# Performance work log

Hardware: AMD Instinct MI355X
Metric: run time of the kernel (lower is better)

The kernel has to match this reference:

```python
import jax, jax.numpy as jnp
import numpy as np

D_MODEL = 2048
NUM_HEADS = 32
D_HEAD = D_MODEL // NUM_HEADS
L = 2048


def setup_inputs() -> dict:
    key = jax.random.key(0)
    ks = jax.random.split(key, 9)
    s = 0.02  # init scale
    return {
        "X": jax.random.normal(ks[0], (L, D_MODEL), dtype=jnp.float32),
        "Wq_w": jax.random.normal(ks[1], (D_MODEL, D_MODEL), jnp.float32) * s,
        "Wq_b": jax.random.normal(ks[2], (D_MODEL,), jnp.float32) * s,
        "Wk_w": jax.random.normal(ks[3], (D_MODEL, D_MODEL), jnp.float32) * s,
        "Wk_b": jax.random.normal(ks[4], (D_MODEL,), jnp.float32) * s,
        "Wv_w": jax.random.normal(ks[5], (D_MODEL, D_MODEL), jnp.float32) * s,
        "Wv_b": jax.random.normal(ks[6], (D_MODEL,), jnp.float32) * s,
        "Wo_w": jax.random.normal(ks[7], (D_MODEL, D_MODEL), jnp.float32) * s,
        "Wo_b": jax.random.normal(ks[8], (D_MODEL,), jnp.float32) * s,
    }


def reference(X, Wq_w, Wq_b, Wk_w, Wk_b, Wv_w, Wv_b, Wo_w, Wo_b):
    # torch.nn.Linear: y = x @ W.T + b
    seq = X.shape[0]
    Q = (X @ Wq_w.T + Wq_b).reshape(seq, D_HEAD, NUM_HEADS)  # (L, d, h)
    K = (X @ Wk_w.T + Wk_b).reshape(seq, D_HEAD, NUM_HEADS)
    V = (X @ Wv_w.T + Wv_b).reshape(seq, D_HEAD, NUM_HEADS)
    # scores[l, m, h] = sum_d Q[l,d,h] * K[m,d,h]; note scale is sqrt(d_model),
    # faithful to the source (not sqrt(d_head)).
    scores = jnp.einsum('ldh,mdh->lmh', Q, K) / jnp.sqrt(jnp.float32(D_MODEL))
    attn = jax.nn.softmax(scores, axis=1)  # softmax over key axis m
    out = jnp.einsum('lmh,mdh->ldh', attn, V).reshape(seq, D_MODEL)
    return out @ Wo_w.T + Wo_b
```

## Files before the change

kernel.cpp:

```cpp
#include <hip/hip_runtime.h>
#include <hip/hip_bf16.h>
#include <stdint.h>
#include <stddef.h>

#define L_SEQ   2048
#define DM      2048
#define NH      32
#define DH      64
#define QSCALE  0.02209708691207961f
#define MAT_N   (L_SEQ * DM)

typedef __bf16  bf16x8 __attribute__((ext_vector_type(8)));
typedef float   f32x4  __attribute__((ext_vector_type(4)));
typedef __hip_bfloat16 bf16;

__device__ __forceinline__ void gl_lds16(const bf16* g, bf16* l) {
    __builtin_amdgcn_global_load_lds(
        (const __attribute__((address_space(1))) unsigned int*)g,
        (__attribute__((address_space(3))) unsigned int*)l,
        16, 0, 0);
}

__device__ __forceinline__ void conv8s(const float* src, bf16* dst, int i, float sc) {
    float4 a = *(const float4*)(src + i);
    float4 b = *(const float4*)(src + i + 4);
    union { bf16 h[8]; uint4 u; } pk;
    pk.h[0] = __float2bfloat16(a.x * sc); pk.h[1] = __float2bfloat16(a.y * sc);
    pk.h[2] = __float2bfloat16(a.z * sc); pk.h[3] = __float2bfloat16(a.w * sc);
    pk.h[4] = __float2bfloat16(b.x * sc); pk.h[5] = __float2bfloat16(b.y * sc);
    pk.h[6] = __float2bfloat16(b.z * sc); pk.h[7] = __float2bfloat16(b.w * sc);
    *(uint4*)(dst + i) = pk.u;
}

__global__ __launch_bounds__(256)
void convert4_kernel(const float* __restrict__ s0, const float* __restrict__ s1,
                     const float* __restrict__ s2, const float* __restrict__ s3,
                     bf16* __restrict__ d0, bf16* __restrict__ d1,
                     bf16* __restrict__ d2, bf16* __restrict__ d3)
{
    const float* s; bf16* d; float sc = 1.0f;
    switch (blockIdx.y) {
        case 0:  s = s0; d = d0; break;
        case 1:  s = s1; d = d1; sc = QSCALE; break;
        case 2:  s = s2; d = d2; break;
        default: s = s3; d = d3; break;
    }
    const int i = (blockIdx.x * 256 + threadIdx.x) * 8;
    conv8s(s, d, i, sc);
}

__global__ __launch_bounds__(256)
void convert_wo_perm_kernel(const float* __restrict__ s, bf16* __restrict__ d)
{
    const int t   = blockIdx.x * 256 + threadIdx.x;
    const int row = t >> 8;
    const int k0  = (t & 255) * 8;
    const float* sr = s + (size_t)row * DM;
    union { bf16 h[8]; uint4 u; } pk;
#pragma unroll
    for (int j = 0; j < 8; ++j) {
        const int kp = k0 + j;
        const int k  = ((kp & 63) << 5) | (kp >> 6);
        pk.h[j] = __float2bfloat16(sr[k]);
    }
    *(uint4*)(d + (size_t)row * DM + k0) = pk.u;
}

__global__ __launch_bounds__(512)
void qkv8_gemm_kernel(const bf16* __restrict__ Xb,
                      const bf16* __restrict__ Wq, const float* __restrict__ bq,
                      const bf16* __restrict__ Wk, const float* __restrict__ bk,
                      const bf16* __restrict__ Wv, const float* __restrict__ bv,
                      bf16* __restrict__ Qws, bf16* __restrict__ Kws, bf16* __restrict__ Vws)
{
    __shared__ bf16 lds[2 * 32768];

    const int bid = blockIdx.x;
    const int mt  = bid & 7;
    const int nt  = bid >> 3;
    const int m0  = mt << 8;
    const int ng0 = nt << 8;
    const int z   = ng0 >> 11;
    const int n0  = ng0 & 2047;
    const bf16*  W    = (z == 0) ? Wq : (z == 1) ? Wk : Wv;
    const float* bias = (z == 0) ? bq : (z == 1) ? bk : bv;

    const int tid  = threadIdx.x;
    const int lane = tid & 63;
    const int wave = tid >> 6;
    const int wm   = wave >> 2;
    const int wn   = wave & 3;
    const int grp8 = (lane >> 4) * 8;
    const int grp4 = (lane >> 4) * 4;
    const int l15  = lane & 15;
    const int axor = (l15 & 7) << 3;

    const int scol = ((tid & 7) * 8) ^ (((tid >> 3) & 7) << 3);
    const bf16* gb[8];
    int loff[8];
#pragma unroll
    for (int e = 0; e < 8; ++e) {
        const int hh  = e >> 1;
        const int row = (e & 1) * 64 + (tid >> 3);
        loff[e] = hh * 8192 + (e & 1) * 4096 + tid * 8;
        if (hh < 2) {
            gb[e] = Xb + (size_t)(m0 + hh * 128 + row) * DM + scol;
        } else {
            const int nn   = n0 + (hh - 2) * 128 + row;
            const int brow = ((nn & 63) << 5) | (nn >> 6);
            gb[e] = W + (size_t)brow * DM + scol;
        }
    }

    const bool swap  = (z == 2);
    const int  aside = swap ? 16384 : 0;
    const int  bside = swap ? 0 : 16384;
    const bf16* fa0 = lds + aside + wm * 8192 + l15 * 64;
    const bf16* fb0 = lds + bside + (wn >> 1) * 8192 + ((wn & 1) * 64 + l15) * 64;

    f32x4 acc[8][4];
    const f32x4 zero = {0.f, 0.f, 0.f, 0.f};
#pragma unroll
    for (int i = 0; i < 8; ++i)
#pragma unroll
        for (int j = 0; j < 4; ++j) acc[i][j] = zero;

#pragma unroll
    for (int e = 0; e < 8; ++e) gl_lds16(gb[e],      lds + loff[e]);
#pragma unroll
    for (int e = 0; e < 8; ++e) gl_lds16(gb[e] + 64, lds + 32768 + loff[e]);
    asm volatile("s_waitcnt vmcnt(8)" ::: "memory");
    asm volatile("s_barrier" ::: "memory");

    for (int t = 0; t < 32; ++t) {
        const int cb = (t & 1) << 15;
        const bf16* fa = fa0 + cb;
        const bf16* fb = fb0 + cb;
        const int c0 = grp8 ^ axor;
        const int c1 = (32 + grp8) ^ axor;

        bf16x8 af[8], bfr[4];
#pragma unroll
        for (int i = 0; i < 8; ++i) af[i] = *(const bf16x8*)(fa + i * 1024 + c0);
#pragma unroll
        for (int j = 0; j < 4; ++j) bfr[j] = *(const bf16x8*)(fb + j * 1024 + c0);
        asm volatile("s_barrier" ::: "memory");
        __builtin_amdgcn_s_setprio(1);
#pragma unroll
        for (int i = 0; i < 8; ++i)
#pragma unroll
            for (int j = 0; j < 4; ++j)
                acc[i][j] = __builtin_amdgcn_mfma_f32_16x16x32_bf16(af[i], bfr[j], acc[i][j], 0, 0, 0);
        __builtin_amdgcn_s_setprio(0);

#pragma unroll
        for (int i = 0; i < 8; ++i) af[i] = *(const bf16x8*)(fa + i * 1024 + c1);
#pragma unroll
        for (int j = 0; j < 4; ++j) bfr[j] = *(const bf16x8*)(fb + j * 1024 + c1);
        asm volatile("s_waitcnt lgkmcnt(0)" ::: "memory");
        asm volatile("s_barrier" ::: "memory");
        if (t + 2 < 32) {
            const int kb2 = (t + 2) << 6;
#pragma unroll
            for (int e = 0; e < 8; ++e)
                gl_lds16(gb[e] + kb2, lds + cb + loff[e]);
            asm volatile("s_waitcnt vmcnt(8)" ::: "memory");
        } else if (t == 30) {
            asm volatile("s_waitcnt vmcnt(0)" ::: "memory");
        }
        __builtin_amdgcn_s_setprio(1);
#pragma unroll
        for (int i = 0; i < 8; ++i)
#pragma unroll
            for (int j = 0; j < 4; ++j)
                acc[i][j] = __builtin_amdgcn_mfma_f32_16x16x32_bf16(af[i], bfr[j], acc[i][j], 0, 0, 0);
        __builtin_amdgcn_s_setprio(0);
        asm volatile("s_barrier" ::: "memory");
    }

    if (z == 0) {
#pragma unroll
        for (int j = 0; j < 4; ++j) {
            const int np = n0 + wn * 64 + j * 16 + l15;
            const float bb = bias[((np & 63) << 5) | (np >> 6)] * QSCALE;
            const size_t base = ((size_t)(np >> 6) * L_SEQ) * DH + (np & 63);
#pragma unroll
            for (int i = 0; i < 8; ++i)
#pragma unroll
                for (int r = 0; r < 4; ++r) {
                    const int m = m0 + wm * 128 + i * 16 + grp4 + r;
                    Qws[base + (size_t)m * DH] = __float2bfloat16(acc[i][j][r] + bb);
                }
        }
    } else if (z == 1) {
#pragma unroll
        for (int j = 0; j < 4; ++j) {
            const int np = n0 + wn * 64 + j * 16 + l15;
            const float bb = bias[((np & 63) << 5) | (np >> 6)];
            const size_t base = ((size_t)(np >> 6) * L_SEQ) * DH + (np & 63);
#pragma unroll
            for (int i = 0; i < 8; ++i)
#pragma unroll
                for (int r = 0; r < 4; ++r) {
                    const int m = m0 + wm * 128 + i * 16 + grp4 + r;
                    Kws[base + (size_t)m * DH] = __float2bfloat16(acc[i][j][r] + bb);
                }
        }
    } else {
#pragma unroll
        for (int i = 0; i < 8; ++i)
#pragma unroll
            for (int r = 0; r < 4; ++r) {
                const int np = n0 + wm * 128 + i * 16 + grp4 + r;
                const float bb = bias[((np & 63) << 5) | (np >> 6)];
#pragma unroll
                for (int j = 0; j < 4; ++j) {
                    const int mcol = m0 + wn * 64 + j * 16 + l15;
                    Vws[(size_t)np * L_SEQ + mcol] = __float2bfloat16(acc[i][j][r] + bb);
                }
            }
    }
}

template<bool PERM>
__device__ __forceinline__ void gemm_mainloop(const bf16* __restrict__ A,
                                              const bf16* __restrict__ B,
                                              int m0, int n0, int kb0, int kb1,
                                              bf16* lds_a, bf16* lds_b,
                                              const bf16* fa, const bf16* fb,
                                              f32x4 acc[4][4])
{
    const int tid  = threadIdx.x;
    const int lane = tid & 63;
    const int wave = tid >> 6;
    const int wr   = (wave >> 1) * 64;
    const int wc   = (wave & 1) * 64;
    const int grp8 = (lane >> 4) * 8;
    const int l15  = lane & 15;

    for (int kb = kb0; kb < kb1; kb += 64) {
        __syncthreads();
#pragma unroll
        for (int r = 0; r < 4; ++r) {
            const int idx = r * 256 + tid;
            const int row = idx >> 3;
            const int col = (idx & 7) * 8;
            gl_lds16(A + (size_t)(m0 + row) * DM + kb + col, lds_a + idx * 8);
            int brow;
            if (PERM) { const int n = n0 + row; brow = ((n & 63) << 5) | (n >> 6); }
            else      { brow = n0 + row; }
            gl_lds16(B + (size_t)brow * DM + kb + col, lds_b + idx * 8);
        }
        __syncthreads();
#pragma unroll
        for (int ks = 0; ks < 2; ++ks) {
            bf16x8 af[4], bfr[4];
#pragma unroll
            for (int i = 0; i < 4; ++i)
                af[i] = *(const bf16x8*)(fa + (wr + i * 16 + l15) * 64 + ks * 32 + grp8);
#pragma unroll
            for (int j = 0; j < 4; ++j)
                bfr[j] = *(const bf16x8*)(fb + (wc + j * 16 + l15) * 64 + ks * 32 + grp8);
#pragma unroll
            for (int i = 0; i < 4; ++i)
#pragma unroll
                for (int j = 0; j < 4; ++j)
                    acc[i][j] = __builtin_amdgcn_mfma_f32_16x16x32_bf16(af[i], bfr[j], acc[i][j], 0, 0, 0);
        }
    }
}

__global__ __launch_bounds__(256)
void out_gemm_splitk_kernel(const bf16* __restrict__ A,
                            const bf16* __restrict__ Wo,
                            float* __restrict__ P0, float* __restrict__ P1)
{
    __shared__ bf16 lds_a[128 * 64];
    __shared__ bf16 lds_b[128 * 64];
    const int m0 = blockIdx.y * 128, n0 = blockIdx.x * 128;
    const int kz = blockIdx.z;
    float* P = kz ? P1 : P0;

    const f32x4 zero = {0.f, 0.f, 0.f, 0.f};
    f32x4 acc[4][4];
#pragma unroll
    for (int i = 0; i < 4; ++i)
#pragma unroll
        for (int j = 0; j < 4; ++j) acc[i][j] = zero;

    gemm_mainloop<false>(A, Wo, m0, n0, kz * (DM / 2), kz * (DM / 2) + DM / 2,
                         lds_a, lds_b, lds_a, lds_b, acc);

    const int lane = threadIdx.x & 63;
    const int wave = threadIdx.x >> 6;
    const int wr = (wave >> 1) * 64, wc = (wave & 1) * 64;
    const int grp4 = (lane >> 4) * 4, l15 = lane & 15;

#pragma unroll
    for (int j = 0; j < 4; ++j) {
        const int n = n0 + wc + j * 16 + l15;
#pragma unroll
        for (int i = 0; i < 4; ++i) {
#pragma unroll
            for (int r = 0; r < 4; ++r) {
                const int m = m0 + wr + i * 16 + grp4 + r;
                P[(size_t)m * DM + n] = acc[i][j][r];
            }
        }
    }
}

__global__ __launch_bounds__(256)
void bias_sum_kernel(const float* __restrict__ P0, const float* __restrict__ P1,
                     const float* __restrict__ bo, float* __restrict__ out)
{
    const int i = (blockIdx.x * 256 + threadIdx.x) * 4;
    float4 a = *(const float4*)(P0 + i);
    float4 b = *(const float4*)(P1 + i);
    float4 c = *(const float4*)(bo + (i & (DM - 1)));
    float4 o;
    o.x = a.x + b.x + c.x; o.y = a.y + b.y + c.y;
    o.z = a.z + b.z + c.z; o.w = a.w + b.w + c.w;
    *(float4*)(out + i) = o;
}

__global__ __launch_bounds__(256)
void attention_kernel(const bf16* __restrict__ Qws,
                      const bf16* __restrict__ Kws,
                      const bf16* __restrict__ Vws,
                      bf16* __restrict__ Attn)
{
    __shared__ bf16 Klds[64 * 72];
    __shared__ bf16 Vlds[64 * 72];
    __shared__ bf16 Plds[64 * 72];

    const int h = blockIdx.x, qb = blockIdx.y;
    const int tid = threadIdx.x;
    const int wave = tid >> 6;
    const int lane = tid & 63;
    const int grp = lane >> 4;
    const int l15 = lane & 15;

    const bf16* Qh = Qws + (size_t)h * L_SEQ * DH;
    const bf16* Kh = Kws + (size_t)h * L_SEQ * DH;
    const bf16* Vh = Vws + (size_t)h * DH * L_SEQ;

    const int q0 = qb * 64 + wave * 16;

    bf16x8 qf0 = *(const bf16x8*)(Qh + (size_t)(q0 + l15) * DH + grp * 8);
    bf16x8 qf1 = *(const bf16x8*)(Qh + (size_t)(q0 + l15) * DH + 32 + grp * 8);

    const f32x4 zero = {0.f, 0.f, 0.f, 0.f};
    f32x4 Oacc[4];
#pragma unroll
    for (int t = 0; t < 4; ++t) Oacc[t] = zero;
    float lsum = 0.f;

    for (int kb = 0; kb < L_SEQ / 64; ++kb) {
        __syncthreads();
#pragma unroll
        for (int rr = 0; rr < 2; ++rr) {
            const int idx = rr * 256 + tid;
            const int row = idx >> 3;
            const int col = (idx & 7) * 8;
            uint4 kv = *(const uint4*)(Kh + (size_t)(kb * 64 + row) * DH + col);
            *(uint4*)(&Klds[row * 72 + col]) = kv;
            uint4 vv = *(const uint4*)(Vh + (size_t)row * L_SEQ + kb * 64 + col);
            *(uint4*)(&Vlds[row * 72 + col]) = vv;
        }
        __syncthreads();

#pragma unroll
        for (int t = 0; t < 4; ++t) {
            bf16x8 k0 = *(const bf16x8*)(&Klds[(t * 16 + l15) * 72 + grp * 8]);
            bf16x8 k1 = *(const bf16x8*)(&Klds[(t * 16 + l15) * 72 + 32 + grp * 8]);
            f32x4 s = zero;
            s = __builtin_amdgcn_mfma_f32_16x16x32_bf16(k0, qf0, s, 0, 0, 0);
            s = __builtin_amdgcn_mfma_f32_16x16x32_bf16(k1, qf1, s, 0, 0, 0);
            float p0 = __expf(s[0]), p1 = __expf(s[1]),
                  p2 = __expf(s[2]), p3 = __expf(s[3]);
            lsum += (p0 + p1) + (p2 + p3);
            union { bf16 hh[4]; uint2 u; } pk;
            pk.hh[0] = __float2bfloat16(p0); pk.hh[1] = __float2bfloat16(p1);
            pk.hh[2] = __float2bfloat16(p2); pk.hh[3] = __float2bfloat16(p3);
            *(uint2*)(&Plds[((size_t)wave * 16 + l15) * 72 + t * 16 + grp * 4]) = pk.u;
        }

        asm volatile("s_waitcnt lgkmcnt(0)" ::: "memory");

#pragma unroll
        for (int ks = 0; ks < 2; ++ks) {
            bf16x8 pa = *(const bf16x8*)(&Plds[(wave * 16 + l15) * 72 + ks * 32 + grp * 8]);
#pragma unroll
            for (int t = 0; t < 4; ++t) {
                bf16x8 vb = *(const bf16x8*)(&Vlds[(t * 16 + l15) * 72 + ks * 32 + grp * 8]);
                Oacc[t] = __builtin_amdgcn_mfma_f32_16x16x32_bf16(pa, vb, Oacc[t], 0, 0, 0);
            }
        }
    }

    float s = lsum;
    s += __shfl_xor(s, 16, 64);
    s += __shfl_xor(s, 32, 64);
    const float inv = 1.f / s;
    float invs[4];
#pragma unroll
    for (int r = 0; r < 4; ++r)
        invs[r] = __shfl(inv, grp * 4 + r, 64);

#pragma unroll
    for (int t = 0; t < 4; ++t) {
#pragma unroll
        for (int r = 0; r < 4; ++r) {
            const int m = q0 + grp * 4 + r;
            const int d = t * 16 + l15;
            Attn[(size_t)m * DM + h * 64 + d] = __float2bfloat16(Oacc[t][r] * invs[r]);
        }
    }
}

extern "C" void kernel_launch(void* const* d_in, const int* in_sizes, int n_in,
                              void* d_out, int out_size, void* d_ws, size_t ws_size,
                              hipStream_t stream)
{
    const float* X  = (const float*)d_in[0];
    const float* Wq = (const float*)d_in[1];
    const float* bq = (const float*)d_in[2];
    const float* Wk = (const float*)d_in[3];
    const float* bk = (const float*)d_in[4];
    const float* Wv = (const float*)d_in[5];
    const float* bv = (const float*)d_in[6];
    const float* Wo = (const float*)d_in[7];
    const float* bo = (const float*)d_in[8];
    float* out = (float*)d_out;

    bf16* Xb   = (bf16*)d_ws;
    bf16* Wqb  = Xb  + (size_t)MAT_N;
    bf16* Wkb  = Wqb + (size_t)MAT_N;
    bf16* Wvb  = Wkb + (size_t)MAT_N;
    bf16* Qws  = Wvb + (size_t)MAT_N;
    bf16* Kws  = Qws + (size_t)MAT_N;
    bf16* Vws  = Kws + (size_t)MAT_N;
    bf16* Wob  = Xb;
    bf16* Attn = Wqb;
    float* P0  = (float*)Wkb;
    float* P1  = (float*)Qws;

    convert4_kernel<<<dim3(2048, 4), 256, 0, stream>>>(X, Wq, Wk, Wv, Xb, Wqb, Wkb, Wvb);
    qkv8_gemm_kernel<<<dim3(192), 512, 0, stream>>>(Xb, Wqb, bq, Wkb, bk, Wvb, bv,
                                                    Qws, Kws, Vws);
    convert_wo_perm_kernel<<<dim3(2048), 256, 0, stream>>>(Wo, Wob);
    attention_kernel<<<dim3(32, 32), 256, 0, stream>>>(Qws, Kws, Vws, Attn);
    out_gemm_splitk_kernel<<<dim3(16, 16, 2), 256, 0, stream>>>(Attn, Wob, P0, P1);
    bias_sum_kernel<<<dim3(4096), 256, 0, stream>>>(P0, P1, bo, out);
}
```

Measured before the change: 302.7 us.

## Double-buffer attention and output GEMM with async LDS loads and swizzle

The attention kernel now uses 512-thread blocks covering 128 queries each. It double-buffers K/V tiles through direct global-to-LDS loads with an XOR swizzle in place of padding, and uses exp2 with the log2(e) factor folded into the Q scale. The output GEMM gets the same treatment: a double-buffered, swizzled mainloop with loads issued two tiles ahead and priority hints around the MFMA blocks. The aim is to hide global-load latency and cut LDS bank conflicts and transcendental cost, at the price of more LDS per block and tighter barrier sequencing.

New measurement: 263.8 us. 12.8% less time.

```diff
diff --git a/kernel.cpp b/kernel.cpp
--- a/kernel.cpp
+++ b/kernel.cpp
@@ -8,11 +8,18 @@
 #define NH      32
 #define DH      64
 #define QSCALE  0.02209708691207961f
+#define QS2     0.0318793579f
 #define MAT_N   (L_SEQ * DM)
 
 typedef __bf16  bf16x8 __attribute__((ext_vector_type(8)));
 typedef float   f32x4  __attribute__((ext_vector_type(4)));
 typedef __hip_bfloat16 bf16;
+
+#if __has_builtin(__builtin_amdgcn_exp2f)
+#define EXP2F(x) __builtin_amdgcn_exp2f(x)
+#else
+#define EXP2F(x) __expf((x) * 0.6931471805599453f)
+#endif
 
 __device__ __forceinline__ void gl_lds16(const bf16* g, bf16* l) {
     __builtin_amdgcn_global_load_lds(
@@ -41,7 +48,7 @@
     const float* s; bf16* d; float sc = 1.0f;
     switch (blockIdx.y) {
         case 0:  s = s0; d = d0; break;
-        case 1:  s = s1; d = d1; sc = QSCALE; break;
+        case 1:  s = s1; d = d1; sc = QS2; break;
         case 2:  s = s2; d = d2; break;
         default: s = s3; d = d3; break;
     }
@@ -182,7 +189,7 @@
 #pragma unroll
         for (int j = 0; j < 4; ++j) {
             const int np = n0 + wn * 64 + j * 16 + l15;
-            const float bb = bias[((np & 63) << 5) | (np >> 6)] * QSCALE;
+            const float bb = bias[((np & 63) << 5) | (np >> 6)] * QS2;
             const size_t base = ((size_t)(np >> 6) * L_SEQ) * DH + (np & 63);
 #pragma unroll
             for (int i = 0; i < 8; ++i)
@@ -222,79 +229,96 @@
     }
 }
 
-template<bool PERM>
-__device__ __forceinline__ void gemm_mainloop(const bf16* __restrict__ A,
-                                              const bf16* __restrict__ B,
-                                              int m0, int n0, int kb0, int kb1,
-                                              bf16* lds_a, bf16* lds_b,
-                                              const bf16* fa, const bf16* fb,
-                                              f32x4 acc[4][4])
-{
+__global__ __launch_bounds__(256)
+void out8_gemm_kernel(const bf16* __restrict__ A,
+                      const bf16* __restrict__ Wo,
+                      float* __restrict__ P0, float* __restrict__ P1)
+{
+    __shared__ bf16 lds[2 * 16384];
+
+    const int m0 = blockIdx.y * 128, n0 = blockIdx.x * 128;
+    const int kz = blockIdx.z;
+    float* P = kz ? P1 : P0;
+    const int kbase = kz * 1024;
+
     const int tid  = threadIdx.x;
     const int lane = tid & 63;
     const int wave = tid >> 6;
     const int wr   = (wave >> 1) * 64;
     const int wc   = (wave & 1) * 64;
     const int grp8 = (lane >> 4) * 8;
+    const int grp4 = (lane >> 4) * 4;
     const int l15  = lane & 15;
-
-    for (int kb = kb0; kb < kb1; kb += 64) {
-        __syncthreads();
-#pragma unroll
-        for (int r = 0; r < 4; ++r) {
-            const int idx = r * 256 + tid;
-            const int row = idx >> 3;
-            const int col = (idx & 7) * 8;
-            gl_lds16(A + (size_t)(m0 + row) * DM + kb + col, lds_a + idx * 8);
-            int brow;
-            if (PERM) { const int n = n0 + row; brow = ((n & 63) << 5) | (n >> 6); }
-            else      { brow = n0 + row; }
-            gl_lds16(B + (size_t)brow * DM + kb + col, lds_b + idx * 8);
-        }
-        __syncthreads();
-#pragma unroll
-        for (int ks = 0; ks < 2; ++ks) {
-            bf16x8 af[4], bfr[4];
-#pragma unroll
-            for (int i = 0; i < 4; ++i)
-                af[i] = *(const bf16x8*)(fa + (wr + i * 16 + l15) * 64 + ks * 32 + grp8);
+    const int axor = (l15 & 7) << 3;
+
+    const bf16* gb[8]; int loff[8];
+#pragma unroll
+    for (int e = 0; e < 8; ++e) {
+        const int idx = (e & 3) * 256 + tid;
+        const int row = idx >> 3;
+        const int sc  = ((idx & 7) * 8) ^ ((row & 7) << 3);
+        if (e < 4) { gb[e] = A  + (size_t)(m0 + row) * DM + kbase + sc; loff[e] = idx * 8; }
+        else       { gb[e] = Wo + (size_t)(n0 + row) * DM + kbase + sc; loff[e] = 8192 + idx * 8; }
+    }
+
+    f32x4 acc[4][4];
+    const f32x4 zero = {0.f, 0.f, 0.f, 0.f};
+#pragma unroll
+    for (int i = 0; i < 4; ++i)
+#pragma unroll
+        for (int j = 0; j < 4; ++j) acc[i][j] = zero;
+
+#pragma unroll
+    for (int e = 0; e < 8; ++e) gl_lds16(gb[e],      lds + loff[e]);
+#pragma unroll
+    for (int e = 0; e < 8; ++e) gl_lds16(gb[e] + 64, lds + 16384 + loff[e]);
+    asm volatile("s_waitcnt vmcnt(8)" ::: "memory");
+    asm volatile("s_barrier" ::: "memory");
+
+    for (int t = 0; t < 16; ++t) {
+        const int cb = (t & 1) << 14;
+        const bf16* fa = lds + cb;
+        const bf16* fb = lds + cb + 8192;
+        const int c0 = grp8 ^ axor;
+        const int c1 = (32 + grp8) ^ axor;
+
+        bf16x8 af[4], bfr[4];
+#pragma unroll
+        for (int i = 0; i < 4; ++i) af[i]  = *(const bf16x8*)(fa + (wr + i * 16 + l15) * 64 + c0);
+#pragma unroll
+        for (int j = 0; j < 4; ++j) bfr[j] = *(const bf16x8*)(fb + (wc + j * 16 + l15) * 64 + c0);
+        asm volatile("s_barrier" ::: "memory");
+        __builtin_amdgcn_s_setprio(1);
+#pragma unroll
+        for (int i = 0; i < 4; ++i)
 #pragma unroll
             for (int j = 0; j < 4; ++j)
-                bfr[j] = *(const bf16x8*)(fb + (wc + j * 16 + l15) * 64 + ks * 32 + grp8);
-#pragma unroll
-            for (int i = 0; i < 4; ++i)
-#pragma unroll
-                for (int j = 0; j < 4; ++j)
-                    acc[i][j] = __builtin_amdgcn_mfma_f32_16x16x32_bf16(af[i], bfr[j], acc[i][j], 0, 0, 0);
-        }
-    }
-}
-
-__global__ __launch_bounds__(256)
-void out_gemm_splitk_kernel(const bf16* __restrict__ A,
-                            const bf16* __restrict__ Wo,
-                            float* __restrict__ P0, float* __restrict__ P1)
-{
-    __shared__ bf16 lds_a[128 * 64];
-    __shared__ bf16 lds_b[128 * 64];
-    const int m0 = blockIdx.y * 128, n0 = blockIdx.x * 128;
-    const int kz = blockIdx.z;
-    float* P = kz ? P1 : P0;
-
-    const f32x4 zero = {0.f, 0.f, 0.f, 0.f};
-    f32x4 acc[4][4];
-#pragma unroll
-    for (int i = 0; i < 4; ++i)
-#pragma unroll
-        for (int j = 0; j < 4; ++j) acc[i][j] = zero;
-
-    gemm_mainloop<false>(A, Wo, m0, n0, kz * (DM / 2), kz * (DM / 2) + DM / 2,
-                         lds_a, lds_b, lds_a, lds_b, acc);
-
-    const int lane = threadIdx.x & 63;
-    const int wave = threadIdx.x >> 6;
-    const int wr = (wave >> 1) * 64, wc = (wave & 1) * 64;
-    const int grp4 = (lane >> 4) * 4, l15 = lane & 15;
+                acc[i][j] = __builtin_amdgcn_mfma_f32_16x16x32_bf16(af[i], bfr[j], acc[i][j], 0, 0, 0);
+        __builtin_amdgcn_s_setprio(0);
+
+#pragma unroll
+        for (int i = 0; i < 4; ++i) af[i]  = *(const bf16x8*)(fa + (wr + i * 16 + l15) * 64 + c1);
+#pragma unroll
+        for (int j = 0; j < 4; ++j) bfr[j] = *(const bf16x8*)(fb + (wc + j * 16 + l15) * 64 + c1);
+        asm volatile("s_waitcnt lgkmcnt(0)" ::: "memory");
+        asm volatile("s_barrier" ::: "memory");
+        if (t + 2 < 16) {
+            const int kadv = (t + 2) * 64;
+#pragma unroll
+            for (int e = 0; e < 8; ++e) gl_lds16(gb[e] + kadv, lds + cb + loff[e]);
+            asm volatile("s_waitcnt vmcnt(8)" ::: "memory");
+        } else if (t == 14) {
+            asm volatile("s_waitcnt vmcnt(0)" ::: "memory");
+        }
+        __builtin_amdgcn_s_setprio(1);
+#pragma unroll
+        for (int i = 0; i < 4; ++i)
+#pragma unroll
+            for (int j = 0; j < 4; ++j)
+                acc[i][j] = __builtin_amdgcn_mfma_f32_16x16x32_bf16(af[i], bfr[j], acc[i][j], 0, 0, 0);
+        __builtin_amdgcn_s_setprio(0);
+        asm volatile("s_barrier" ::: "memory");
+    }
 
 #pragma unroll
     for (int j = 0; j < 4; ++j) {
@@ -324,31 +348,40 @@
     *(float4*)(out + i) = o;
 }
 
-__global__ __launch_bounds__(256)
+__global__ __launch_bounds__(512)
 void attention_kernel(const bf16* __restrict__ Qws,
                       const bf16* __restrict__ Kws,
                       const bf16* __restrict__ Vws,
                       bf16* __restrict__ Attn)
 {
-    __shared__ bf16 Klds[64 * 72];
-    __shared__ bf16 Vlds[64 * 72];
-    __shared__ bf16 Plds[64 * 72];
+    __shared__ bf16 lds[24576];
 
     const int h = blockIdx.x, qb = blockIdx.y;
-    const int tid = threadIdx.x;
+    const int tid  = threadIdx.x;
     const int wave = tid >> 6;
     const int lane = tid & 63;
-    const int grp = lane >> 4;
-    const int l15 = lane & 15;
+    const int grp  = lane >> 4;
+    const int l15  = lane & 15;
+    const int grp8 = grp * 8;
+    const int axor = (l15 & 7) << 3;
 
     const bf16* Qh = Qws + (size_t)h * L_SEQ * DH;
     const bf16* Kh = Kws + (size_t)h * L_SEQ * DH;
     const bf16* Vh = Vws + (size_t)h * DH * L_SEQ;
 
-    const int q0 = qb * 64 + wave * 16;
-
-    bf16x8 qf0 = *(const bf16x8*)(Qh + (size_t)(q0 + l15) * DH + grp * 8);
-    bf16x8 qf1 = *(const bf16x8*)(Qh + (size_t)(q0 + l15) * DH + 32 + grp * 8);
+    const int q0 = qb * 128 + wave * 16;
+
+    bf16x8 qf0 = *(const bf16x8*)(Qh + (size_t)(q0 + l15) * DH + grp8);
+    bf16x8 qf1 = *(const bf16x8*)(Qh + (size_t)(q0 + l15) * DH + 32 + grp8);
+
+    const int srow = tid >> 3;
+    const int scol = ((tid & 7) * 8) ^ ((srow & 7) << 3);
+    const bf16* gK = Kh + (size_t)srow * DH + scol;
+    const bf16* gV = Vh + (size_t)srow * L_SEQ + scol;
+    bf16* ldsK = lds + tid * 8;
+    bf16* ldsV = lds + 8192 + tid * 8;
+    bf16* Plds = lds + 16384;
+    const int prow = (wave * 16 + l15) * 64;
 
     const f32x4 zero = {0.f, 0.f, 0.f, 0.f};
     f32x4 Oacc[4];
@@ -356,53 +389,66 @@
     for (int t = 0; t < 4; ++t) Oacc[t] = zero;
     float lsum = 0.f;
 
-    for (int kb = 0; kb < L_SEQ / 64; ++kb) {
-        __syncthreads();
-#pragma unroll
-        for (int rr = 0; rr < 2; ++rr) {
-            const int idx = rr * 256 + tid;
-            const int row = idx >> 3;
-            const int col = (idx & 7) * 8;
-            uint4 kv = *(const uint4*)(Kh + (size_t)(kb * 64 + row) * DH + col);
-            *(uint4*)(&Klds[row * 72 + col]) = kv;
-            uint4 vv = *(const uint4*)(Vh + (size_t)row * L_SEQ + kb * 64 + col);
-            *(uint4*)(&Vlds[row * 72 + col]) = vv;
-        }
-        __syncthreads();
+    gl_lds16(gK,        ldsK);
+    gl_lds16(gV,        ldsV);
+    gl_lds16(gK + 4096, ldsK + 4096);
+    gl_lds16(gV + 64,   ldsV + 4096);
+    asm volatile("s_waitcnt vmcnt(2)" ::: "memory");
+    asm volatile("s_barrier" ::: "memory");
+
+    for (int kb = 0; kb < 32; ++kb) {
+        const int cb = (kb & 1) << 12;
+        const bf16* Kc = lds + cb;
+        const bf16* Vc = lds + 8192 + cb;
 
 #pragma unroll
         for (int t = 0; t < 4; ++t) {
-            bf16x8 k0 = *(const bf16x8*)(&Klds[(t * 16 + l15) * 72 + grp * 8]);
-            bf16x8 k1 = *(const bf16x8*)(&Klds[(t * 16 + l15) * 72 + 32 + grp * 8]);
+            const int rr = (t * 16 + l15) * 64;
+            bf16x8 k0 = *(const bf16x8*)(Kc + rr + (grp8 ^ axor));
+            bf16x8 k1 = *(const bf16x8*)(Kc + rr + ((32 + grp8) ^ axor));
             f32x4 s = zero;
+            __builtin_amdgcn_s_setprio(1);
             s = __builtin_amdgcn_mfma_f32_16x16x32_bf16(k0, qf0, s, 0, 0, 0);
             s = __builtin_amdgcn_mfma_f32_16x16x32_bf16(k1, qf1, s, 0, 0, 0);
-            float p0 = __expf(s[0]), p1 = __expf(s[1]),
-                  p2 = __expf(s[2]), p3 = __expf(s[3]);
+            __builtin_amdgcn_s_setprio(0);
+            float p0 = EXP2F(s[0]), p1 = EXP2F(s[1]),
+                  p2 = EXP2F(s[2]), p3 = EXP2F(s[3]);
             lsum += (p0 + p1) + (p2 + p3);
             union { bf16 hh[4]; uint2 u; } pk;
             pk.hh[0] = __float2bfloat16(p0); pk.hh[1] = __float2bfloat16(p1);
             pk.hh[2] = __float2bfloat16(p2); pk.hh[3] = __float2bfloat16(p3);
-            *(uint2*)(&Plds[((size_t)wave * 16 + l15) * 72 + t * 16 + grp * 4]) = pk.u;
-        }
-
+            *(uint2*)(&Plds[prow + ((t * 16 + grp * 4) ^ axor)]) = pk.u;
+        }
         asm volatile("s_waitcnt lgkmcnt(0)" ::: "memory");
 
+        __builtin_amdgcn_s_setprio(1);
 #pragma unroll
         for (int ks = 0; ks < 2; ++ks) {
-            bf16x8 pa = *(const bf16x8*)(&Plds[(wave * 16 + l15) * 72 + ks * 32 + grp * 8]);
+            bf16x8 pa = *(const bf16x8*)(&Plds[prow + ((ks * 32 + grp8) ^ axor)]);
 #pragma unroll
             for (int t = 0; t < 4; ++t) {
-                bf16x8 vb = *(const bf16x8*)(&Vlds[(t * 16 + l15) * 72 + ks * 32 + grp * 8]);
+                bf16x8 vb = *(const bf16x8*)(Vc + (t * 16 + l15) * 64 + ((ks * 32 + grp8) ^ axor));
                 Oacc[t] = __builtin_amdgcn_mfma_f32_16x16x32_bf16(pa, vb, Oacc[t], 0, 0, 0);
             }
         }
-    }
-
-    float s = lsum;
-    s += __shfl_xor(s, 16, 64);
-    s += __shfl_xor(s, 32, 64);
-    const float inv = 1.f / s;
+        __builtin_amdgcn_s_setprio(0);
+
+        asm volatile("s_waitcnt lgkmcnt(0)" ::: "memory");
+        asm volatile("s_barrier" ::: "memory");
+        if (kb + 2 < 32) {
+            gl_lds16(gK + (kb + 2) * 4096, ldsK + cb);
+            gl_lds16(gV + (kb + 2) * 64,   ldsV + cb);
+            asm volatile("s_waitcnt vmcnt(2)" ::: "memory");
+        } else if (kb == 30) {
+            asm volatile("s_waitcnt vmcnt(0)" ::: "memory");
+        }
+        asm volatile("s_barrier" ::: "memory");
+    }
+
+    float sden = lsum;
+    sden += __shfl_xor(sden, 16, 64);
+    sden += __shfl_xor(sden, 32, 64);
+    const float inv = 1.f / sden;
     float invs[4];
 #pragma unroll
     for (int r = 0; r < 4; ++r)
@@ -450,7 +496,7 @@
     qkv8_gemm_kernel<<<dim3(192), 512, 0, stream>>>(Xb, Wqb, bq, Wkb, bk, Wvb, bv,
                                                     Qws, Kws, Vws);
     convert_wo_perm_kernel<<<dim3(2048), 256, 0, stream>>>(Wo, Wob);
-    attention_kernel<<<dim3(32, 32), 256, 0, stream>>>(Qws, Kws, Vws, Attn);
-    out_gemm_splitk_kernel<<<dim3(16, 16, 2), 256, 0, stream>>>(Attn, Wob, P0, P1);
+    attention_kernel<<<dim3(32, 16), 512, 0, stream>>>(Qws, Kws, Vws, Attn);
+    out8_gemm_kernel<<<dim3(16, 16, 2), 256, 0, stream>>>(Attn, Wob, P0, P1);
     bias_sum_kernel<<<dim3(4096), 256, 0, stream>>>(P0, P1, bo, out);
 }
```
